# Optimization experiments

Measured on AMD Instinct MI355X. Metric: run time of the kernel, lower is better.

Reference implementation:

```python
import jax, jax.numpy as jnp
import numpy as np

N_NODES = 50000
NUM_GRAPHS = 64
HID = 128
OUT = 128
NUM_LAYERS = 4


def _glorot(key, shape):
    fan_in, fan_out = shape[0], shape[1]
    lim = float(np.sqrt(6.0 / (fan_in + fan_out)))
    return jax.random.uniform(key, shape, jnp.float32, -lim, lim)


def setup_inputs() -> dict:
    key = jax.random.key(0)
    ks = jax.random.split(key, 16)
    x = jax.random.normal(ks[0], (N_NODES, HID), jnp.float32)
    edge_index = jax.random.randint(ks[1], (2, 640000), 0, N_NODES, jnp.int64)
    batch = jnp.sort(jax.random.randint(ks[2], (N_NODES,), 0, NUM_GRAPHS, jnp.int64))
    W_in = _glorot(ks[3], (HID, HID))
    b_in = jnp.zeros((HID,), jnp.float32)
    conv_W = jnp.stack([_glorot(ks[4 + i], (HID, HID)) for i in range(NUM_LAYERS)])
    conv_b = jnp.zeros((NUM_LAYERS, HID), jnp.float32)
    W_def = _glorot(ks[8], (HID, OUT)); b_def = jnp.zeros((OUT,), jnp.float32)
    W_syn = _glorot(ks[9], (HID, OUT)); b_syn = jnp.zeros((OUT,), jnp.float32)
    W_rel = _glorot(ks[10], (HID, OUT)); b_rel = jnp.zeros((OUT,), jnp.float32)
    return {"x": x, "edge_index": edge_index, "batch": batch,
            "W_in": W_in, "b_in": b_in, "conv_W": conv_W, "conv_b": conv_b,
            "W_def": W_def, "b_def": b_def, "W_syn": W_syn, "b_syn": b_syn,
            "W_rel": W_rel, "b_rel": b_rel}


def _gcn_norm(edge_index, n_nodes):
    # add self-loops, symmetric degree normalization (PyG gcn_norm defaults)
    loops = jnp.arange(n_nodes, dtype=edge_index.dtype)
    row = jnp.concatenate([edge_index[0], loops])  # source
    col = jnp.concatenate([edge_index[1], loops])  # target (aggregation index)
    deg = jax.ops.segment_sum(jnp.ones_like(col, jnp.float32), col, num_segments=n_nodes)
    dinv = jnp.where(deg > 0, jax.lax.rsqrt(jnp.maximum(deg, 1.0)), 0.0)
    norm = dinv[row] * dinv[col]  # [E+N]
    return row, col, norm


def _gcn_conv(h, row, col, norm, W, b, n_nodes):
    h = h @ W
    msg = h[row] * norm[:, None]            # gather from source, scale
    agg = jax.ops.segment_sum(msg, col, num_segments=n_nodes)  # scatter-add to target
    return agg + b


def reference(x, edge_index, batch, W_in, b_in, conv_W, conv_b,
              W_def, b_def, W_syn, b_syn, W_rel, b_rel):
    n = x.shape[0]
    row, col, norm = _gcn_norm(edge_index, n)
    h = jax.nn.relu(x @ W_in + b_in)  # dropout is identity in eval mode
    for i in range(NUM_LAYERS):
        h = jax.nn.relu(_gcn_conv(h, row, col, norm, conv_W[i], conv_b[i], n))
    # global mean pool over graphs
    sums = jax.ops.segment_sum(h, batch, num_segments=NUM_GRAPHS)
    cnts = jax.ops.segment_sum(jnp.ones((n,), jnp.float32), batch, num_segments=NUM_GRAPHS)
    pooled = sums / jnp.maximum(cnts, 1.0)[:, None]
    out_def = pooled @ W_def + b_def
    out_syn = pooled @ W_syn + b_syn
    out_rel = pooled @ W_rel + b_rel
    return (out_def, out_syn, out_rel)
```

## Files before the change

### kernel.cpp

```cpp
#include <hip/hip_runtime.h>
#include <hip/hip_bf16.h>

#define N_NODES 50000
#define NGRAPH 64
#define HID 128
#define NLAYERS 4
#define SCAN_NB ((N_NODES + 511) / 512)
#define HIST_NB 2500
#define WPREP_NB 320

typedef __attribute__((ext_vector_type(8))) __bf16 bf16x8;
typedef __attribute__((ext_vector_type(8))) unsigned short ushort8;
typedef __attribute__((ext_vector_type(4))) float f32x4;

__device__ __forceinline__ float bf2f(unsigned short u) { return __uint_as_float(((unsigned)u) << 16); }
__device__ __forceinline__ unsigned short f2bf(float f) { return __hip_bfloat16_raw(__float2bfloat16(f)).x; }
__device__ __forceinline__ float ulo(unsigned m) { return __uint_as_float(m << 16); }
__device__ __forceinline__ float uhi(unsigned m) { return __uint_as_float(m & 0xffff0000u); }

__global__ void k_init(int* __restrict__ cnt, int* __restrict__ gstart, int* __restrict__ gend) {
  int i = blockIdx.x * blockDim.x + threadIdx.x;
  if (i < N_NODES) cnt[i] = 0;
  if (i < NGRAPH) { gstart[i] = 0; gend[i] = 0; }
}

__global__ void k_hist(const int* __restrict__ col, int E, int* __restrict__ cnt,
                       const int* __restrict__ batch, int* __restrict__ gstart, int* __restrict__ gend,
                       const float* __restrict__ Win, const float* __restrict__ Wconv,
                       unsigned short* __restrict__ WtAll) {
  if (blockIdx.x < HIST_NB) {
    int e = blockIdx.x * blockDim.x + threadIdx.x;
    if (e < E) atomicAdd(&cnt[col[e]], 1);
    if (e < N_NODES) {
      int b = batch[e];
      if (e == 0 || batch[e - 1] != b) gstart[b] = e;
      if (e == N_NODES - 1 || batch[e + 1] != b) gend[b] = e + 1;
    }
  } else {
    int idx = (blockIdx.x - HIST_NB) * 256 + threadIdx.x;
    if (idx >= 5 * HID * HID) return;
    int m = idx >> 14, rem = idx & 16383;
    int k = rem >> 7, n = rem & 127;
    const float* src = (m == 0) ? Win : (Wconv + (size_t)(m - 1) * HID * HID);
    WtAll[(size_t)m * HID * HID + n * HID + k] = f2bf(src[k * HID + n]);
  }
}

__global__ __launch_bounds__(512) void k_scan1(const int* __restrict__ cnt, int* __restrict__ excl,
                                               int* __restrict__ bsum) {
  __shared__ int tmp[512];
  const int t = threadIdx.x;
  const int i = blockIdx.x * 512 + t;
  int v = (i < N_NODES) ? cnt[i] : 0;
  tmp[t] = v;
  __syncthreads();
#pragma unroll
  for (int off = 1; off < 512; off <<= 1) {
    int u = (t >= off) ? tmp[t - off] : 0;
    __syncthreads();
    tmp[t] += u;
    __syncthreads();
  }
  if (i < N_NODES) excl[i] = tmp[t] - v;
  if (t == 511) bsum[blockIdx.x] = tmp[511];
}

__global__ __launch_bounds__(128) void k_scan2(int* __restrict__ bsum, int* __restrict__ offs) {
  __shared__ int tmp[128];
  const int t = threadIdx.x;
  int v = (t < SCAN_NB) ? bsum[t] : 0;
  tmp[t] = v;
  __syncthreads();
#pragma unroll
  for (int off = 1; off < 128; off <<= 1) {
    int u = (t >= off) ? tmp[t - off] : 0;
    __syncthreads();
    tmp[t] += u;
    __syncthreads();
  }
  if (t < SCAN_NB) bsum[t] = tmp[t] - v;
  if (t == 127) offs[N_NODES] = tmp[127];
}

__global__ __launch_bounds__(512) void k_scan3(const int* __restrict__ cnt, const int* __restrict__ excl,
                                               const int* __restrict__ bsum, int* __restrict__ offs,
                                               int* __restrict__ cursor, float* __restrict__ dinv) {
  const int i = blockIdx.x * 512 + threadIdx.x;
  if (i >= N_NODES) return;
  int o = excl[i] + bsum[blockIdx.x];
  offs[i] = o;
  cursor[i] = o;
  dinv[i] = 1.0f / sqrtf((float)(cnt[i] + 1));
}

__global__ void k_fill(const int* __restrict__ row, const int* __restrict__ col, int E,
                       int* __restrict__ cursor, unsigned short* __restrict__ csr_src) {
  int e = blockIdx.x * blockDim.x + threadIdx.x;
  if (e >= E) return;
  int pos = atomicAdd(&cursor[col[e]], 1);
  csr_src[pos] = (unsigned short)row[e];
}

template <bool AF32, bool BIAS, bool RELU, bool SCALE>
__global__ __launch_bounds__(256) void k_gemm_mfma(const void* __restrict__ Av,
                                                   const unsigned short* __restrict__ Wt,
                                                   const float* __restrict__ bias,
                                                   const float* __restrict__ dinv,
                                                   unsigned short* __restrict__ Y, int M) {
  __shared__ float ys[64][132];
  const int wave = threadIdx.x >> 6;
  const int lane = threadIdx.x & 63;
  const int row16 = (blockIdx.x * 4 + wave) * 16;
  const int lr = lane & 15;
  const int lk = (lane >> 4) * 8;

  f32x4 acc[8];
#pragma unroll
  for (int i = 0; i < 8; ++i) acc[i] = (f32x4){0.f, 0.f, 0.f, 0.f};

  const int arow = min(row16 + lr, M - 1);
#pragma unroll
  for (int ks = 0; ks < 4; ++ks) {
    const int k0 = ks * 32 + lk;
    bf16x8 a;
    if (AF32) {
      const float* Af = (const float*)Av;
      float4 f0 = *(const float4*)(Af + (size_t)arow * HID + k0);
      float4 f1 = *(const float4*)(Af + (size_t)arow * HID + k0 + 4);
      ushort8 u;
      u[0] = f2bf(f0.x); u[1] = f2bf(f0.y); u[2] = f2bf(f0.z); u[3] = f2bf(f0.w);
      u[4] = f2bf(f1.x); u[5] = f2bf(f1.y); u[6] = f2bf(f1.z); u[7] = f2bf(f1.w);
      a = __builtin_bit_cast(bf16x8, u);
    } else {
      const unsigned short* Ab = (const unsigned short*)Av;
      a = *(const bf16x8*)(Ab + (size_t)arow * HID + k0);
    }
#pragma unroll
    for (int nt = 0; nt < 8; ++nt) {
      bf16x8 b = *(const bf16x8*)(Wt + (size_t)(nt * 16 + lr) * HID + k0);
      acc[nt] = __builtin_amdgcn_mfma_f32_16x16x32_bf16(a, b, acc[nt], 0, 0, 0);
    }
  }

  const int wrow = wave * 16 + (lane >> 4) * 4;
#pragma unroll
  for (int nt = 0; nt < 8; ++nt) {
    const int c = nt * 16 + lr;
#pragma unroll
    for (int r = 0; r < 4; ++r) ys[wrow + r][c] = acc[nt][r];
  }
  __syncthreads();

  const int er = threadIdx.x >> 2;
  const int q = threadIdx.x & 3;
  const int grow = blockIdx.x * 64 + er;
  if (grow < M) {
    float scale = SCALE ? dinv[grow] : 1.f;
    ushort8 pk[4];
#pragma unroll
    for (int h = 0; h < 4; ++h) {
#pragma unroll
      for (int j = 0; j < 8; ++j) {
        int c = q * 32 + h * 8 + j;
        float v = ys[er][c];
        if (BIAS) v += bias[c];
        if (RELU) v = fmaxf(v, 0.f);
        if (SCALE) v *= scale;
        pk[h][j] = f2bf(v);
      }
    }
    unsigned short* dst = Y + (size_t)grow * HID + q * 32;
    *(ushort8*)(dst)      = pk[0];
    *(ushort8*)(dst + 8)  = pk[1];
    *(ushort8*)(dst + 16) = pk[2];
    *(ushort8*)(dst + 24) = pk[3];
  }
}

__global__ __launch_bounds__(256) void k_agg(const unsigned short* __restrict__ g, const int* __restrict__ offs,
                                             const unsigned short* __restrict__ csr_src,
                                             const float* __restrict__ dinv,
                                             const float* __restrict__ bias, unsigned short* __restrict__ out) {
  const int wave = threadIdx.x >> 6;
  const int lane = threadIdx.x & 63;
  const int v = blockIdx.x * 4 + wave;
  if (v >= N_NODES) return;
  const int s = lane >> 4;
  const int c = lane & 15;

  const uint4* g4 = (const uint4*)g;

  float a0 = 0.f, a1 = 0.f, a2 = 0.f, a3 = 0.f, a4 = 0.f, a5 = 0.f, a6 = 0.f, a7 = 0.f;
  if (s == 0) {
    uint4 m = g4[(size_t)v * 16 + c];
    a0 = ulo(m.x); a1 = uhi(m.x); a2 = ulo(m.y); a3 = uhi(m.y);
    a4 = ulo(m.z); a5 = uhi(m.z); a6 = ulo(m.w); a7 = uhi(m.w);
  }

  const int lo = offs[v], hi = offs[v + 1];
  int idx = lo + s;
  for (; idx + 4 < hi; idx += 8) {
    int s0 = csr_src[idx];
    int s1 = csr_src[idx + 4];
    uint4 m0 = g4[(size_t)s0 * 16 + c];
    uint4 m1 = g4[(size_t)s1 * 16 + c];
    a0 += ulo(m0.x) + ulo(m1.x); a1 += uhi(m0.x) + uhi(m1.x);
    a2 += ulo(m0.y) + ulo(m1.y); a3 += uhi(m0.y) + uhi(m1.y);
    a4 += ulo(m0.z) + ulo(m1.z); a5 += uhi(m0.z) + uhi(m1.z);
    a6 += ulo(m0.w) + ulo(m1.w); a7 += uhi(m0.w) + uhi(m1.w);
  }
  if (idx < hi) {
    uint4 m0 = g4[(size_t)csr_src[idx] * 16 + c];
    a0 += ulo(m0.x); a1 += uhi(m0.x);
    a2 += ulo(m0.y); a3 += uhi(m0.y);
    a4 += ulo(m0.z); a5 += uhi(m0.z);
    a6 += ulo(m0.w); a7 += uhi(m0.w);
  }

  a0 += __shfl_xor(a0, 16, 64); a0 += __shfl_xor(a0, 32, 64);
  a1 += __shfl_xor(a1, 16, 64); a1 += __shfl_xor(a1, 32, 64);
  a2 += __shfl_xor(a2, 16, 64); a2 += __shfl_xor(a2, 32, 64);
  a3 += __shfl_xor(a3, 16, 64); a3 += __shfl_xor(a3, 32, 64);
  a4 += __shfl_xor(a4, 16, 64); a4 += __shfl_xor(a4, 32, 64);
  a5 += __shfl_xor(a5, 16, 64); a5 += __shfl_xor(a5, 32, 64);
  a6 += __shfl_xor(a6, 16, 64); a6 += __shfl_xor(a6, 32, 64);
  a7 += __shfl_xor(a7, 16, 64); a7 += __shfl_xor(a7, 32, 64);

  if (s == 0) {
    const float d = dinv[v];
    float4 b0 = ((const float4*)bias)[c * 2];
    float4 b1 = ((const float4*)bias)[c * 2 + 1];
    float o0 = fmaxf(d * a0 + b0.x, 0.f), o1 = fmaxf(d * a1 + b0.y, 0.f);
    float o2 = fmaxf(d * a2 + b0.z, 0.f), o3 = fmaxf(d * a3 + b0.w, 0.f);
    float o4 = fmaxf(d * a4 + b1.x, 0.f), o5 = fmaxf(d * a5 + b1.y, 0.f);
    float o6 = fmaxf(d * a6 + b1.z, 0.f), o7 = fmaxf(d * a7 + b1.w, 0.f);
    uint4 pk;
    pk.x = (unsigned)f2bf(o0) | ((unsigned)f2bf(o1) << 16);
    pk.y = (unsigned)f2bf(o2) | ((unsigned)f2bf(o3) << 16);
    pk.z = (unsigned)f2bf(o4) | ((unsigned)f2bf(o5) << 16);
    pk.w = (unsigned)f2bf(o6) | ((unsigned)f2bf(o7) << 16);
    ((uint4*)out)[(size_t)v * 16 + c] = pk;
  }
}

__global__ __launch_bounds__(512) void k_agggemm(const unsigned short* __restrict__ g,
                                                 const int* __restrict__ offs,
                                                 const unsigned short* __restrict__ csr_src,
                                                 const float* __restrict__ dinv,
                                                 const float* __restrict__ bias,
                                                 const unsigned short* __restrict__ Wt,
                                                 unsigned short* __restrict__ gout) {
  __shared__ unsigned short hs[64][136];
  const int wid = threadIdx.x >> 6;
  const int lane = threadIdx.x & 63;
  const int s = lane >> 4;
  const int c = lane & 15;
  const int tile = blockIdx.x * 64;
  const uint4* g4 = (const uint4*)g;

  for (int it = 0; it < 8; ++it) {
    const int vloc = wid * 8 + it;
    const int v = tile + vloc;
    if (v >= N_NODES) break;

    float a0 = 0.f, a1 = 0.f, a2 = 0.f, a3 = 0.f, a4 = 0.f, a5 = 0.f, a6 = 0.f, a7 = 0.f;
    if (s == 0) {
      uint4 m = g4[(size_t)v * 16 + c];
      a0 = ulo(m.x); a1 = uhi(m.x); a2 = ulo(m.y); a3 = uhi(m.y);
      a4 = ulo(m.z); a5 = uhi(m.z); a6 = ulo(m.w); a7 = uhi(m.w);
    }
    const int lo = offs[v], hi = offs[v + 1];
    int idx = lo + s;
    for (; idx + 4 < hi; idx += 8) {
      int s0 = csr_src[idx];
      int s1 = csr_src[idx + 4];
      uint4 m0 = g4[(size_t)s0 * 16 + c];
      uint4 m1 = g4[(size_t)s1 * 16 + c];
      a0 += ulo(m0.x) + ulo(m1.x); a1 += uhi(m0.x) + uhi(m1.x);
      a2 += ulo(m0.y) + ulo(m1.y); a3 += uhi(m0.y) + uhi(m1.y);
      a4 += ulo(m0.z) + ulo(m1.z); a5 += uhi(m0.z) + uhi(m1.z);
      a6 += ulo(m0.w) + ulo(m1.w); a7 += uhi(m0.w) + uhi(m1.w);
    }
    if (idx < hi) {
      uint4 m0 = g4[(size_t)csr_src[idx] * 16 + c];
      a0 += ulo(m0.x); a1 += uhi(m0.x);
      a2 += ulo(m0.y); a3 += uhi(m0.y);
      a4 += ulo(m0.z); a5 += uhi(m0.z);
      a6 += ulo(m0.w); a7 += uhi(m0.w);
    }
    a0 += __shfl_xor(a0, 16, 64); a0 += __shfl_xor(a0, 32, 64);
    a1 += __shfl_xor(a1, 16, 64); a1 += __shfl_xor(a1, 32, 64);
    a2 += __shfl_xor(a2, 16, 64); a2 += __shfl_xor(a2, 32, 64);
    a3 += __shfl_xor(a3, 16, 64); a3 += __shfl_xor(a3, 32, 64);
    a4 += __shfl_xor(a4, 16, 64); a4 += __shfl_xor(a4, 32, 64);
    a5 += __shfl_xor(a5, 16, 64); a5 += __shfl_xor(a5, 32, 64);
    a6 += __shfl_xor(a6, 16, 64); a6 += __shfl_xor(a6, 32, 64);
    a7 += __shfl_xor(a7, 16, 64); a7 += __shfl_xor(a7, 32, 64);

    if (s == 0) {
      const float d = dinv[v];
      float4 b0 = ((const float4*)bias)[c * 2];
      float4 b1 = ((const float4*)bias)[c * 2 + 1];
      float o0 = fmaxf(d * a0 + b0.x, 0.f), o1 = fmaxf(d * a1 + b0.y, 0.f);
      float o2 = fmaxf(d * a2 + b0.z, 0.f), o3 = fmaxf(d * a3 + b0.w, 0.f);
      float o4 = fmaxf(d * a4 + b1.x, 0.f), o5 = fmaxf(d * a5 + b1.y, 0.f);
      float o6 = fmaxf(d * a6 + b1.z, 0.f), o7 = fmaxf(d * a7 + b1.w, 0.f);
      uint4 pk;
      pk.x = (unsigned)f2bf(o0) | ((unsigned)f2bf(o1) << 16);
      pk.y = (unsigned)f2bf(o2) | ((unsigned)f2bf(o3) << 16);
      pk.z = (unsigned)f2bf(o4) | ((unsigned)f2bf(o5) << 16);
      pk.w = (unsigned)f2bf(o6) | ((unsigned)f2bf(o7) << 16);
      *(uint4*)&hs[vloc][c * 8] = pk;
    }
  }
  __syncthreads();

  const int mt = wid & 3;
  const int nb = (wid >> 2) * 4;
  const int lr = lane & 15;
  const int lk = (lane >> 4) * 8;

  f32x4 acc[4];
#pragma unroll
  for (int j = 0; j < 4; ++j) acc[j] = (f32x4){0.f, 0.f, 0.f, 0.f};

#pragma unroll
  for (int ks = 0; ks < 4; ++ks) {
    const int k0 = ks * 32 + lk;
    bf16x8 a = *(const bf16x8*)&hs[mt * 16 + lr][k0];
#pragma unroll
    for (int j = 0; j < 4; ++j) {
      bf16x8 b = *(const bf16x8*)(Wt + (size_t)((nb + j) * 16 + lr) * HID + k0);
      acc[j] = __builtin_amdgcn_mfma_f32_16x16x32_bf16(a, b, acc[j], 0, 0, 0);
    }
  }

  const int drow = tile + mt * 16 + (lane >> 4) * 4;
#pragma unroll
  for (int j = 0; j < 4; ++j) {
    const int gcol = (nb + j) * 16 + lr;
#pragma unroll
    for (int r = 0; r < 4; ++r) {
      const int rr = drow + r;
      if (rr < N_NODES) gout[(size_t)rr * HID + gcol] = f2bf(acc[j][r] * dinv[rr]);
    }
  }
}

__global__ __launch_bounds__(1024) void k_poolheads(const unsigned short* __restrict__ h,
                                                    const int* __restrict__ gstart, const int* __restrict__ gend,
                                                    const float* __restrict__ W0, const float* __restrict__ b0,
                                                    const float* __restrict__ W1, const float* __restrict__ b1,
                                                    const float* __restrict__ W2, const float* __restrict__ b2,
                                                    float* __restrict__ out) {
  __shared__ float red[1024];
  __shared__ float pm[HID];
  const int g = blockIdx.x;
  const int tid = threadIdx.x;
  const int j = tid & 127;
  const int r0 = tid >> 7;
  const int lo = gstart[g], hi = gend[g];
  float acc = 0.f;
  for (int v = lo + r0; v < hi; v += 8) acc += bf2f(h[(size_t)v * HID + j]);
  red[tid] = acc;
  __syncthreads();
  if (r0 < 4) red[tid] += red[tid + 512];
  __syncthreads();
  if (r0 < 2) red[tid] += red[tid + 256];
  __syncthreads();
  if (r0 < 1) {
    float s = red[tid] + red[tid + 128];
    pm[j] = s / fmaxf((float)(hi - lo), 1.f);
  }
  __syncthreads();
  if (tid < 384) {
    const int t = tid >> 7;
    const int cc = tid & 127;
    const float* W = (t == 0) ? W0 : ((t == 1) ? W1 : W2);
    const float* b = (t == 0) ? b0 : ((t == 1) ? b1 : b2);
    float a2 = 0.f;
#pragma unroll 8
    for (int k = 0; k < HID; ++k) a2 += pm[k] * W[k * HID + cc];
    out[((size_t)t * NGRAPH + g) * HID + cc] = a2 + b[cc];
  }
}

extern "C" void kernel_launch(void* const* d_in, const int* in_sizes, int n_in,
                              void* d_out, int out_size, void* d_ws, size_t ws_size,
                              hipStream_t stream) {
  const float* x     = (const float*)d_in[0];
  const int*   ei    = (const int*)d_in[1];
  const int*   batch = (const int*)d_in[2];
  const float* W_in  = (const float*)d_in[3];
  const float* b_in  = (const float*)d_in[4];
  const float* convW = (const float*)d_in[5];
  const float* convb = (const float*)d_in[6];
  const float* W_def = (const float*)d_in[7];
  const float* b_def = (const float*)d_in[8];
  const float* W_syn = (const float*)d_in[9];
  const float* b_syn = (const float*)d_in[10];
  const float* W_rel = (const float*)d_in[11];
  const float* b_rel = (const float*)d_in[12];

  const int E = in_sizes[1] / 2;
  const int* row = ei;
  const int* col = ei + E;

  char* base = (char*)d_ws;
  size_t off = 0;
  auto alloc = [&](size_t bytes) -> void* {
    void* p = base + off;
    off += (bytes + 255) & ~size_t(255);
    return p;
  };
  int*   cnt     = (int*)  alloc((size_t)N_NODES * 4);
  float* dinv    = (float*)alloc((size_t)N_NODES * 4);
  int*   offs    = (int*)  alloc((size_t)(N_NODES + 1) * 4);
  int*   cursor  = (int*)  alloc((size_t)N_NODES * 4);
  int*   excl    = (int*)  alloc((size_t)N_NODES * 4);
  int*   bsum    = (int*)  alloc((size_t)SCAN_NB * 4);
  unsigned short* csr_src = (unsigned short*)alloc((size_t)E * 2);
  unsigned short* hA = (unsigned short*)alloc((size_t)N_NODES * HID * 2);
  unsigned short* hB = (unsigned short*)alloc((size_t)N_NODES * HID * 2);
  unsigned short* hC = (unsigned short*)alloc((size_t)N_NODES * HID * 2);
  unsigned short* WtAll = (unsigned short*)alloc((size_t)5 * HID * HID * 2);
  int*   gstart  = (int*)  alloc((size_t)NGRAPH * 4);
  int*   gend    = (int*)  alloc((size_t)NGRAPH * 4);

  k_init<<<(N_NODES + 255) / 256, 256, 0, stream>>>(cnt, gstart, gend);
  k_hist<<<HIST_NB + WPREP_NB, 256, 0, stream>>>(col, E, cnt, batch, gstart, gend, W_in, convW, WtAll);
  k_scan1<<<SCAN_NB, 512, 0, stream>>>(cnt, excl, bsum);
  k_scan2<<<1, 128, 0, stream>>>(bsum, offs);
  k_scan3<<<SCAN_NB, 512, 0, stream>>>(cnt, excl, bsum, offs, cursor, dinv);
  k_fill<<<(E + 255) / 256, 256, 0, stream>>>(row, col, E, cursor, csr_src);

  const int gemm_grid = (N_NODES + 63) / 64;
  k_gemm_mfma<true, true, true, false><<<gemm_grid, 256, 0, stream>>>(x, WtAll, b_in, nullptr, hA, N_NODES);
  k_gemm_mfma<false, false, false, true><<<gemm_grid, 256, 0, stream>>>(
      hA, WtAll + (size_t)1 * HID * HID, nullptr, dinv, hB, N_NODES);

  unsigned short* gin = hB;
  unsigned short* gout = hC;
  for (int i = 0; i < 3; ++i) {
    k_agggemm<<<gemm_grid, 512, 0, stream>>>(gin, offs, csr_src, dinv,
                                             convb + (size_t)i * HID,
                                             WtAll + (size_t)(i + 2) * HID * HID, gout);
    unsigned short* t = gin; gin = gout; gout = t;
  }

  k_agg<<<(N_NODES + 3) / 4, 256, 0, stream>>>(gin, offs, csr_src, dinv,
                                               convb + (size_t)3 * HID, hA);

  k_poolheads<<<NGRAPH, 1024, 0, stream>>>(hA, gstart, gend, W_def, b_def, W_syn, b_syn, W_rel, b_rel,
                                           (float*)d_out);
}
```

Baseline: 326.1 us.

## Fuse input projection and first conv GEMM into one kernel via LDS

Replaces the two back-to-back GEMM launches (input linear with bias+ReLU, then first conv weight with dinv scaling) with a single 512-thread kernel. The intermediate 64-row tile is kept in shared memory as bf16, so it is never written to or re-read from global memory, and one launch is removed. Each wave now computes a 16x64 slice instead of 16x128, so the B operand loads are split across two wave groups. The final store writes scalar bf16 values per lane rather than packed 16-byte rows, which may make global writes less efficient.

Result: no change. 320.3 us (-1.8%).

```diff
diff --git a/kernel.cpp b/kernel.cpp
--- a/kernel.cpp
+++ b/kernel.cpp
@@ -101,79 +101,74 @@
   csr_src[pos] = (unsigned short)row[e];
 }
 
-template <bool AF32, bool BIAS, bool RELU, bool SCALE>
-__global__ __launch_bounds__(256) void k_gemm_mfma(const void* __restrict__ Av,
-                                                   const unsigned short* __restrict__ Wt,
-                                                   const float* __restrict__ bias,
-                                                   const float* __restrict__ dinv,
-                                                   unsigned short* __restrict__ Y, int M) {
-  __shared__ float ys[64][132];
-  const int wave = threadIdx.x >> 6;
+__global__ __launch_bounds__(512) void k_gemm01(const float* __restrict__ x,
+                                                const unsigned short* __restrict__ Wt0,
+                                                const float* __restrict__ b_in,
+                                                const unsigned short* __restrict__ Wt1,
+                                                const float* __restrict__ dinv,
+                                                unsigned short* __restrict__ gout) {
+  __shared__ unsigned short hs[64][136];
+  const int wid = threadIdx.x >> 6;
   const int lane = threadIdx.x & 63;
-  const int row16 = (blockIdx.x * 4 + wave) * 16;
+  const int tile = blockIdx.x * 64;
   const int lr = lane & 15;
   const int lk = (lane >> 4) * 8;
-
-  f32x4 acc[8];
-#pragma unroll
-  for (int i = 0; i < 8; ++i) acc[i] = (f32x4){0.f, 0.f, 0.f, 0.f};
-
-  const int arow = min(row16 + lr, M - 1);
+  const int mt = wid & 3;
+  const int nb = (wid >> 2) * 4;
+
+  f32x4 acc[4];
+#pragma unroll
+  for (int j = 0; j < 4; ++j) acc[j] = (f32x4){0.f, 0.f, 0.f, 0.f};
+
+  const int arow = min(tile + mt * 16 + lr, N_NODES - 1);
 #pragma unroll
   for (int ks = 0; ks < 4; ++ks) {
     const int k0 = ks * 32 + lk;
-    bf16x8 a;
-    if (AF32) {
-      const float* Af = (const float*)Av;
-      float4 f0 = *(const float4*)(Af + (size_t)arow * HID + k0);
-      float4 f1 = *(const float4*)(Af + (size_t)arow * HID + k0 + 4);
-      ushort8 u;
-      u[0] = f2bf(f0.x); u[1] = f2bf(f0.y); u[2] = f2bf(f0.z); u[3] = f2bf(f0.w);
-      u[4] = f2bf(f1.x); u[5] = f2bf(f1.y); u[6] = f2bf(f1.z); u[7] = f2bf(f1.w);
-      a = __builtin_bit_cast(bf16x8, u);
-    } else {
-      const unsigned short* Ab = (const unsigned short*)Av;
-      a = *(const bf16x8*)(Ab + (size_t)arow * HID + k0);
-    }
-#pragma unroll
-    for (int nt = 0; nt < 8; ++nt) {
-      bf16x8 b = *(const bf16x8*)(Wt + (size_t)(nt * 16 + lr) * HID + k0);
-      acc[nt] = __builtin_amdgcn_mfma_f32_16x16x32_bf16(a, b, acc[nt], 0, 0, 0);
-    }
-  }
-
-  const int wrow = wave * 16 + (lane >> 4) * 4;
-#pragma unroll
-  for (int nt = 0; nt < 8; ++nt) {
-    const int c = nt * 16 + lr;
-#pragma unroll
-    for (int r = 0; r < 4; ++r) ys[wrow + r][c] = acc[nt][r];
-  }
-  __syncthreads();
-
-  const int er = threadIdx.x >> 2;
-  const int q = threadIdx.x & 3;
-  const int grow = blockIdx.x * 64 + er;
-  if (grow < M) {
-    float scale = SCALE ? dinv[grow] : 1.f;
-    ushort8 pk[4];
-#pragma unroll
-    for (int h = 0; h < 4; ++h) {
-#pragma unroll
-      for (int j = 0; j < 8; ++j) {
-        int c = q * 32 + h * 8 + j;
-        float v = ys[er][c];
-        if (BIAS) v += bias[c];
-        if (RELU) v = fmaxf(v, 0.f);
-        if (SCALE) v *= scale;
-        pk[h][j] = f2bf(v);
-      }
-    }
-    unsigned short* dst = Y + (size_t)grow * HID + q * 32;
-    *(ushort8*)(dst)      = pk[0];
-    *(ushort8*)(dst + 8)  = pk[1];
-    *(ushort8*)(dst + 16) = pk[2];
-    *(ushort8*)(dst + 24) = pk[3];
+    float4 f0 = *(const float4*)(x + (size_t)arow * HID + k0);
+    float4 f1 = *(const float4*)(x + (size_t)arow * HID + k0 + 4);
+    ushort8 u;
+    u[0] = f2bf(f0.x); u[1] = f2bf(f0.y); u[2] = f2bf(f0.z); u[3] = f2bf(f0.w);
+    u[4] = f2bf(f1.x); u[5] = f2bf(f1.y); u[6] = f2bf(f1.z); u[7] = f2bf(f1.w);
+    bf16x8 a = __builtin_bit_cast(bf16x8, u);
+#pragma unroll
+    for (int j = 0; j < 4; ++j) {
+      bf16x8 b = *(const bf16x8*)(Wt0 + (size_t)((nb + j) * 16 + lr) * HID + k0);
+      acc[j] = __builtin_amdgcn_mfma_f32_16x16x32_bf16(a, b, acc[j], 0, 0, 0);
+    }
+  }
+  const int drloc = mt * 16 + (lane >> 4) * 4;
+#pragma unroll
+  for (int j = 0; j < 4; ++j) {
+    const int gcol = (nb + j) * 16 + lr;
+    const float bv = b_in[gcol];
+#pragma unroll
+    for (int r = 0; r < 4; ++r)
+      hs[drloc + r][gcol] = f2bf(fmaxf(acc[j][r] + bv, 0.f));
+  }
+  __syncthreads();
+
+#pragma unroll
+  for (int j = 0; j < 4; ++j) acc[j] = (f32x4){0.f, 0.f, 0.f, 0.f};
+
+#pragma unroll
+  for (int ks = 0; ks < 4; ++ks) {
+    const int k0 = ks * 32 + lk;
+    bf16x8 a = *(const bf16x8*)&hs[mt * 16 + lr][k0];
+#pragma unroll
+    for (int j = 0; j < 4; ++j) {
+      bf16x8 b = *(const bf16x8*)(Wt1 + (size_t)((nb + j) * 16 + lr) * HID + k0);
+      acc[j] = __builtin_amdgcn_mfma_f32_16x16x32_bf16(a, b, acc[j], 0, 0, 0);
+    }
+  }
+  const int drow = tile + mt * 16 + (lane >> 4) * 4;
+#pragma unroll
+  for (int j = 0; j < 4; ++j) {
+    const int gcol = (nb + j) * 16 + lr;
+#pragma unroll
+    for (int r = 0; r < 4; ++r) {
+      const int rr = drow + r;
+      if (rr < N_NODES) gout[(size_t)rr * HID + gcol] = f2bf(acc[j][r] * dinv[rr]);
+    }
   }
 }
 
@@ -435,9 +430,7 @@
   k_fill<<<(E + 255) / 256, 256, 0, stream>>>(row, col, E, cursor, csr_src);
 
   const int gemm_grid = (N_NODES + 63) / 64;
-  k_gemm_mfma<true, true, true, false><<<gemm_grid, 256, 0, stream>>>(x, WtAll, b_in, nullptr, hA, N_NODES);
-  k_gemm_mfma<false, false, false, true><<<gemm_grid, 256, 0, stream>>>(
-      hA, WtAll + (size_t)1 * HID * HID, nullptr, dinv, hB, N_NODES);
+  k_gemm01<<<gemm_grid, 512, 0, stream>>>(x, WtAll, b_in, WtAll + (size_t)1 * HID * HID, dinv, hB);
 
   unsigned short* gin = hB;
   unsigned short* gout = hC;
```
